# Kernel tuning notes

Hardware: AMD Instinct MI355X
Metric: run time of the kernel (lower is better)

Reference implementation:

```python
import jax, jax.numpy as jnp
import numpy as np

NUM_HEADS = 12
WINDOW = 128


def setup_inputs() -> dict:
    key = jax.random.key(0)
    k1, k2, k3, k4 = jax.random.split(key, 4)
    B, S, E = 2, 4096, 768
    x = jax.random.normal(k1, (B, S, E), dtype=jnp.float32)
    # nn.MultiheadAttention parameters
    w_in = jax.random.normal(k2, (3 * E, E), dtype=jnp.float32) * 0.02   # in_proj_weight
    b_in = jnp.zeros((3 * E,), dtype=jnp.float32)                        # in_proj_bias
    w_out = jax.random.normal(k3, (E, E), dtype=jnp.float32) * 0.02      # out_proj.weight
    b_out = jnp.zeros((E,), dtype=jnp.float32)                           # out_proj.bias
    return {"x": x, "w_in": w_in, "b_in": b_in, "w_out": w_out, "b_out": b_out}


def reference(x, w_in, b_in, w_out, b_out):
    B, S, E = x.shape
    H = NUM_HEADS
    D = E // H
    # fused qkv projection: x @ w_in.T + b_in -> [B, S, 3E]
    qkv = jnp.einsum('bse,fe->bsf', x, w_in) + b_in
    q, k, v = jnp.split(qkv, 3, axis=-1)
    q = q.reshape(B, S, H, D).transpose(0, 2, 1, 3)  # [B,H,S,D]
    k = k.reshape(B, S, H, D).transpose(0, 2, 1, 3)
    v = v.reshape(B, S, H, D).transpose(0, 2, 1, 3)
    scale = jnp.asarray(D, x.dtype) ** -0.5
    scores = jnp.einsum('bhqd,bhkd->bhqk', q * scale, k)  # [B,H,S,S]
    # Torch semantics: boolean attn_mask True == NOT allowed. The module sets
    # True inside the +-window band, so the band is masked out.
    idx = jnp.arange(S)
    band = jnp.abs(idx[:, None] - idx[None, :]) <= WINDOW  # True inside window
    scores = jnp.where(band[None, None, :, :], -jnp.inf, scores)
    attn = jax.nn.softmax(scores, axis=-1)
    out = jnp.einsum('bhqk,bhkd->bhqd', attn, v)  # [B,H,S,D]
    out = out.transpose(0, 2, 1, 3).reshape(B, S, E)
    return jnp.einsum('bse,fe->bsf', out, w_out) + b_out
```

## Files before the change

### kernel.cpp

```cpp
#include <hip/hip_runtime.h>
#include <hip/hip_bf16.h>
#include <stdint.h>

typedef __bf16 bf16_t;
typedef __bf16 bf16x8 __attribute__((ext_vector_type(8)));
typedef __bf16 bf16x4v __attribute__((ext_vector_type(4)));
typedef float f32x4 __attribute__((ext_vector_type(4)));

#define DEV __device__ __forceinline__

static constexpr int B_ = 2, S_ = 4096, E_ = 768, H_ = 12, D_ = 64;
static constexpr int WINDOW_ = 128;
static constexpr float QSCALE = 0.125f * 1.44269504088896f;

template<int C> struct IC { static constexpr int v = C; };

DEV float fexp2(float x) { return __builtin_amdgcn_exp2f(x); }

DEV void gload_lds16(const void* g, void* l) {
    __builtin_amdgcn_global_load_lds(
        (const __attribute__((address_space(1))) uint32_t*)g,
        (__attribute__((address_space(3))) uint32_t*)l, 16, 0, 0);
}

__global__ void k_cvt(const float* __restrict__ in, bf16_t* __restrict__ out, int n) {
    int i = (blockIdx.x * blockDim.x + threadIdx.x) * 4;
    if (i < n) {
        float4 v = *(const float4*)(in + i);
        bf16x4v o;
        o[0] = (bf16_t)v.x; o[1] = (bf16_t)v.y; o[2] = (bf16_t)v.z; o[3] = (bf16_t)v.w;
        *(bf16x4v*)(out + i) = o;
    }
}

template<int EPI>
__global__ void k_gemm(const bf16_t* __restrict__ A, const bf16_t* __restrict__ Bw,
                       const float* __restrict__ bias,
                       bf16_t* __restrict__ qb, bf16_t* __restrict__ kb, bf16_t* __restrict__ vtb,
                       float* __restrict__ outf,
                       int M, int N, int K, int mtiles) {
    __shared__ bf16_t As[128 * 64];
    __shared__ bf16_t Bs[128 * 64];
    int bid = blockIdx.x;
    int tm = bid % mtiles, tn = bid / mtiles;
    int m0 = tm * 128, n0 = tn * 128;
    int t = threadIdx.x;
    int lane = t & 63, wid = t >> 6;
    int l15 = lane & 15, l4 = lane >> 4;
    int wm = (wid & 1) * 64, wn = (wid >> 1) * 64;

    f32x4 acc[4][4];
#pragma unroll
    for (int i = 0; i < 4; ++i)
#pragma unroll
        for (int j = 0; j < 4; ++j) acc[i][j] = f32x4{0.f, 0.f, 0.f, 0.f};

    for (int kt = 0; kt < K; kt += 64) {
        __syncthreads();
#pragma unroll
        for (int c = 0; c < 4; ++c) {
            int idx = t + 256 * c;
            int row = idx >> 3, part = idx & 7;
            int kc = 8 * (part ^ (row & 7));
            gload_lds16(A + (long)(m0 + row) * K + kt + kc, (char*)As + idx * 16);
            gload_lds16(Bw + (long)(n0 + row) * K + kt + kc, (char*)Bs + idx * 16);
        }
        __syncthreads();
#pragma unroll
        for (int kk = 0; kk < 2; ++kk) {
            bf16x8 af[4], bfr[4];
#pragma unroll
            for (int i = 0; i < 4; ++i) {
                int row = wm + i * 16 + l15;
                int off = row * 128 + ((16 * (kk * 4 + l4)) ^ ((row & 7) << 4));
                af[i] = *(const bf16x8*)((const char*)As + off);
                int rowb = wn + i * 16 + l15;
                int offb = rowb * 128 + ((16 * (kk * 4 + l4)) ^ ((rowb & 7) << 4));
                bfr[i] = *(const bf16x8*)((const char*)Bs + offb);
            }
#pragma unroll
            for (int i = 0; i < 4; ++i)
#pragma unroll
                for (int j = 0; j < 4; ++j)
                    acc[i][j] = __builtin_amdgcn_mfma_f32_16x16x32_bf16(af[i], bfr[j], acc[i][j], 0, 0, 0);
        }
    }

#pragma unroll
    for (int i = 0; i < 4; ++i) {
#pragma unroll
        for (int j = 0; j < 4; ++j) {
            int n = n0 + wn + j * 16 + l15;
            float bv = bias[n];
            int mbase = m0 + wm + i * 16 + l4 * 4;
            if (EPI == 0) {
                int sel = n / 768, nn = n % 768;
                int h = nn >> 6, d = nn & 63;
                int b = mbase >> 12, s = mbase & 4095;
                if (sel == 2) {
                    bf16x4v pk;
#pragma unroll
                    for (int r = 0; r < 4; ++r) pk[r] = (bf16_t)(acc[i][j][r] + bv);
                    int pos = (s & ~31) | (((s >> 2) & 3) << 3) | (((s >> 4) & 1) << 2);
                    *(bf16x4v*)(vtb + ((long)(b * H_ + h) * D_ + d) * S_ + pos) = pk;
                } else {
                    long o = ((long)(b * H_ + h) * S_ + s) * D_ + d;
#pragma unroll
                    for (int r = 0; r < 4; ++r) {
                        float v = acc[i][j][r] + bv;
                        if (sel == 0) qb[o + (long)r * D_] = (bf16_t)(v * QSCALE);
                        else          kb[o + (long)r * D_] = (bf16_t)v;
                    }
                }
            } else {
#pragma unroll
                for (int r = 0; r < 4; ++r)
                    outf[(long)(mbase + r) * 768 + n] = acc[i][j][r] + bv;
            }
        }
    }
}

__global__ __launch_bounds__(512, 6)
void k_attn(const bf16_t* __restrict__ q, const bf16_t* __restrict__ k,
            const bf16_t* __restrict__ vt, bf16_t* __restrict__ ao) {
    __shared__ bf16_t Ksh[3][4096];
    __shared__ bf16_t Vsh[3][4096];
    int bid = blockIdx.x;
    bid = (bid & 7) * 96 + (bid >> 3);
    int bh = bid >> 5, qt = bid & 31;
    int q0 = qt * 128;
    int b = bh / H_, h = bh % H_;
    int t = threadIdx.x, lane = t & 63, wid = t >> 6;
    int l15 = lane & 15, l4 = lane >> 4;

    const bf16_t* qp = q + (long)bh * S_ * D_;
    const bf16_t* kp = k + (long)bh * S_ * D_;
    const bf16_t* vp = vt + (long)bh * D_ * S_;
    int wq = q0 + wid * 16;

    bf16x8 qf[2];
    {
        int row = wq + l15;
        qf[0] = *(const bf16x8*)(qp + (long)row * 64 + 8 * l4);
        qf[1] = *(const bf16x8*)(qp + (long)row * 64 + 32 + 8 * l4);
    }

    int sw = (l15 & 7) << 4;
    int a0 = l15 * 128 + ((16 * l4) ^ sw);
    int a1 = a0 ^ 64;

    f32x4 o[4], osum;
    osum = f32x4{0.f, 0.f, 0.f, 0.f};
#pragma unroll
    for (int ns = 0; ns < 4; ++ns) o[ns] = f32x4{0.f, 0.f, 0.f, 0.f};
    float m_ = 0.f;
    f32x4 mneg4 = f32x4{0.f, 0.f, 0.f, 0.f};

    bf16x8 onesB;
#pragma unroll
    for (int j = 0; j < 8; ++j) onesB[j] = (bf16_t)1.0f;

    int srow = t >> 3, spart = t & 7;
    int ssw = 8 * (spart ^ (srow & 7));
    int koff = srow * 64 + ssw;
    int voff = srow * S_ + ssw;
    int qt2 = 2 * qt;
    int qg = wq + l15;

    auto NK = [&](int i) { return i < qt2 ? i : i + 2; };

    auto STAGE = [&](int kts, auto bufc) {
        constexpr int buf = decltype(bufc)::v;
        gload_lds16(kp + ((long)kts << 12) + koff, (char*)Ksh + buf * 8192 + t * 16);
        gload_lds16(vp + (kts << 6) + voff, (char*)Vsh + buf * 8192 + t * 16);
    };

    auto QK = [&](auto curc, f32x4* s, f32x4 cinit) {
        constexpr int cur = decltype(curc)::v;
        const char* KL = (const char*)Ksh + cur * 8192;
#pragma unroll
        for (int ks = 0; ks < 4; ++ks) {
            bf16x8 kf0 = *(const bf16x8*)(KL + a0 + ks * 2048);
            bf16x8 kf1 = *(const bf16x8*)(KL + a1 + ks * 2048);
            s[ks] = __builtin_amdgcn_mfma_f32_16x16x32_bf16(kf0, qf[0], cinit, 0, 0, 0);
            s[ks] = __builtin_amdgcn_mfma_f32_16x16x32_bf16(kf1, qf[1], s[ks], 0, 0, 0);
        }
    };

    auto MASK = [&](int kt, f32x4* s) {
        int k0 = kt << 6;
#pragma unroll
        for (int ks = 0; ks < 4; ++ks) {
            int kb_ = k0 + ks * 16 + l4 * 4;
#pragma unroll
            for (int r = 0; r < 4; ++r) {
                int dd = qg - (kb_ + r); int ad = dd < 0 ? -dd : dd;
                if (ad <= WINDOW_) s[ks][r] = -1e30f;
            }
        }
    };

    auto TAIL = [&](auto curc, f32x4* s) {
        constexpr int cur = decltype(curc)::v;
        bf16x8 pa[2];
#pragma unroll
        for (int c = 0; c < 2; ++c) {
            pa[c][0] = (bf16_t)s[2*c][0];   pa[c][1] = (bf16_t)s[2*c][1];
            pa[c][2] = (bf16_t)s[2*c][2];   pa[c][3] = (bf16_t)s[2*c][3];
            pa[c][4] = (bf16_t)s[2*c+1][0]; pa[c][5] = (bf16_t)s[2*c+1][1];
            pa[c][6] = (bf16_t)s[2*c+1][2]; pa[c][7] = (bf16_t)s[2*c+1][3];
        }
        osum = __builtin_amdgcn_mfma_f32_16x16x32_bf16(pa[0], onesB, osum, 0, 0, 0);
        osum = __builtin_amdgcn_mfma_f32_16x16x32_bf16(pa[1], onesB, osum, 0, 0, 0);
        const char* VL = (const char*)Vsh + cur * 8192;
#pragma unroll
        for (int ns = 0; ns < 4; ++ns) {
            bf16x8 vf0 = *(const bf16x8*)(VL + a0 + ns * 2048);
            bf16x8 vf1 = *(const bf16x8*)(VL + a1 + ns * 2048);
            o[ns] = __builtin_amdgcn_mfma_f32_16x16x32_bf16(pa[0], vf0, o[ns], 0, 0, 0);
            o[ns] = __builtin_amdgcn_mfma_f32_16x16x32_bf16(pa[1], vf1, o[ns], 0, 0, 0);
        }
    };

    auto body = [&](int idx, auto curc) {
        if (idx < 61) {
            STAGE(NK(idx + 1), IC<(decltype(curc)::v + 1) % 3>{});
            asm volatile("s_waitcnt vmcnt(2)" ::: "memory");
        } else {
            asm volatile("s_waitcnt vmcnt(0)" ::: "memory");
        }
        __builtin_amdgcn_s_barrier();
        __builtin_amdgcn_sched_barrier(0);

        int kt = NK(idx);
        int dk = kt - qt2;
        f32x4 s[4];
        QK(curc, s, mneg4);
        if (dk == -2 || dk == -1 || dk == 2 || dk == 3) MASK(kt, s);
#pragma unroll
        for (int ks = 0; ks < 4; ++ks)
#pragma unroll
            for (int r = 0; r < 4; ++r)
                s[ks][r] = fexp2(s[ks][r]);
        TAIL(curc, s);
    };

    STAGE(NK(0), IC<0>{});

    {
        STAGE(NK(1), IC<1>{});
        asm volatile("s_waitcnt vmcnt(2)" ::: "memory");
        __builtin_amdgcn_s_barrier();
        __builtin_amdgcn_sched_barrier(0);

        int kt = NK(0);
        int dk = kt - qt2;
        f32x4 s[4];
        QK(IC<0>{}, s, f32x4{0.f, 0.f, 0.f, 0.f});
        if (dk == -2 || dk == -1 || dk == 2 || dk == 3) MASK(kt, s);
        float lm = -1e30f;
#pragma unroll
        for (int ks = 0; ks < 4; ++ks) {
            float a = fmaxf(fmaxf(s[ks][0], s[ks][1]), fmaxf(s[ks][2], s[ks][3]));
            lm = fmaxf(lm, a);
        }
        lm = fmaxf(lm, __shfl_xor(lm, 16));
        lm = fmaxf(lm, __shfl_xor(lm, 32));
        m_ = fmaxf(lm, 0.0f);
        mneg4 = f32x4{-m_, -m_, -m_, -m_};
#pragma unroll
        for (int ks = 0; ks < 4; ++ks)
#pragma unroll
            for (int r = 0; r < 4; ++r)
                s[ks][r] = fexp2(s[ks][r] - m_);
        TAIL(IC<0>{}, s);
    }

    for (int i3 = 0; i3 < 20; ++i3) {
        body(3 * i3 + 1, IC<1>{});
        body(3 * i3 + 2, IC<2>{});
        body(3 * i3 + 3, IC<0>{});
    }
    body(61, IC<1>{});

#pragma unroll
    for (int r = 0; r < 4; ++r) {
        float ir = 1.0f / osum[r];
        int srow2 = wq + l4 * 4 + r;
#pragma unroll
        for (int ns = 0; ns < 4; ++ns) {
            int e = h * 64 + ns * 16 + l15;
            ao[((long)b * S_ + srow2) * E_ + e] = (bf16_t)(o[ns][r] * ir);
        }
    }
}

extern "C" void kernel_launch(void* const* d_in, const int* in_sizes, int n_in,
                              void* d_out, int out_size, void* d_ws, size_t ws_size,
                              hipStream_t stream) {
    const float* x     = (const float*)d_in[0];
    const float* w_in  = (const float*)d_in[1];
    const float* b_in  = (const float*)d_in[2];
    const float* w_out = (const float*)d_in[3];
    const float* b_out = (const float*)d_in[4];
    float* out = (float*)d_out;

    char* ws = (char*)d_ws;
    bf16_t* xb  = (bf16_t*)(ws + 0);
    bf16_t* wib = (bf16_t*)(ws + 12582912);
    bf16_t* wob = (bf16_t*)(ws + 16121856);
    bf16_t* qb  = (bf16_t*)(ws + 17301504);
    bf16_t* kb  = (bf16_t*)(ws + 29884416);
    bf16_t* vtb = (bf16_t*)(ws + 42467328);
    bf16_t* ao  = xb;

    k_cvt<<<6144, 256, 0, stream>>>(x, xb, 6291456);
    k_cvt<<<1728, 256, 0, stream>>>(w_in, wib, 1769472);
    k_cvt<<<576, 256, 0, stream>>>(w_out, wob, 589824);

    k_gemm<0><<<64 * 18, 256, 0, stream>>>(xb, wib, b_in, qb, kb, vtb, nullptr,
                                           8192, 2304, 768, 64);
    k_attn<<<24 * 32, 512, 0, stream>>>(qb, kb, vtb, ao);
    k_gemm<1><<<64 * 6, 256, 0, stream>>>(ao, wob, b_out, nullptr, nullptr, nullptr, out,
                                          8192, 768, 768, 64);
}
```

Before: 189.9 us.

## Switch attention kernel to 32x32x16 MFMA with 4 waves and permlane swaps

Rewrites the windowed-attention kernel to use 32x32x16 bf16 MFMA tiles: each of 4 waves (256 threads) handles 32 query rows instead of 8 waves with 16 rows each. Score-to-P conversion uses permlane32_swap to reshape the accumulator into a B operand without going through LDS, and the V-transpose layout written by the QKV GEMM drops its permuted position encoding to match. The intent is fewer MFMA issues and fewer LDS reads per FLOP, plus vectorized output stores. The cost is higher register pressure from 16-wide accumulators and half the threads per block, each issuing twice the global-to-LDS loads.

Measured after the change: 207.8 us. 9.4% more time.

```diff
diff --git a/kernel.cpp b/kernel.cpp
--- a/kernel.cpp
+++ b/kernel.cpp
@@ -6,6 +6,7 @@
 typedef __bf16 bf16x8 __attribute__((ext_vector_type(8)));
 typedef __bf16 bf16x4v __attribute__((ext_vector_type(4)));
 typedef float f32x4 __attribute__((ext_vector_type(4)));
+typedef float f32x16 __attribute__((ext_vector_type(16)));
 
 #define DEV __device__ __forceinline__
 
@@ -16,6 +17,17 @@
 template<int C> struct IC { static constexpr int v = C; };
 
 DEV float fexp2(float x) { return __builtin_amdgcn_exp2f(x); }
+
+DEV uint32_t pk2(float lo, float hi) {
+    union { bf16_t h[2]; uint32_t u; } r;
+    r.h[0] = (bf16_t)lo; r.h[1] = (bf16_t)hi;
+    return r.u;
+}
+
+DEV void swap32(uint32_t& a, uint32_t& b) {
+    auto r = __builtin_amdgcn_permlane32_swap(a, b, false, false);
+    a = r[0]; b = r[1];
+}
 
 DEV void gload_lds16(const void* g, void* l) {
     __builtin_amdgcn_global_load_lds(
@@ -101,8 +113,7 @@
                     bf16x4v pk;
 #pragma unroll
                     for (int r = 0; r < 4; ++r) pk[r] = (bf16_t)(acc[i][j][r] + bv);
-                    int pos = (s & ~31) | (((s >> 2) & 3) << 3) | (((s >> 4) & 1) << 2);
-                    *(bf16x4v*)(vtb + ((long)(b * H_ + h) * D_ + d) * S_ + pos) = pk;
+                    *(bf16x4v*)(vtb + ((long)(b * H_ + h) * D_ + d) * S_ + s) = pk;
                 } else {
                     long o = ((long)(b * H_ + h) * S_ + s) * D_ + d;
 #pragma unroll
@@ -121,7 +132,7 @@
     }
 }
 
-__global__ __launch_bounds__(512, 6)
+__global__ __launch_bounds__(256, 3)
 void k_attn(const bf16_t* __restrict__ q, const bf16_t* __restrict__ k,
             const bf16_t* __restrict__ vt, bf16_t* __restrict__ ao) {
     __shared__ bf16_t Ksh[3][4096];
@@ -132,101 +143,103 @@
     int q0 = qt * 128;
     int b = bh / H_, h = bh % H_;
     int t = threadIdx.x, lane = t & 63, wid = t >> 6;
-    int l15 = lane & 15, l4 = lane >> 4;
+    int l31 = lane & 31, l5 = lane >> 5;
 
     const bf16_t* qp = q + (long)bh * S_ * D_;
     const bf16_t* kp = k + (long)bh * S_ * D_;
     const bf16_t* vp = vt + (long)bh * D_ * S_;
-    int wq = q0 + wid * 16;
-
-    bf16x8 qf[2];
-    {
-        int row = wq + l15;
-        qf[0] = *(const bf16x8*)(qp + (long)row * 64 + 8 * l4);
-        qf[1] = *(const bf16x8*)(qp + (long)row * 64 + 32 + 8 * l4);
-    }
-
-    int sw = (l15 & 7) << 4;
-    int a0 = l15 * 128 + ((16 * l4) ^ sw);
-    int a1 = a0 ^ 64;
-
-    f32x4 o[4], osum;
-    osum = f32x4{0.f, 0.f, 0.f, 0.f};
-#pragma unroll
-    for (int ns = 0; ns < 4; ++ns) o[ns] = f32x4{0.f, 0.f, 0.f, 0.f};
-    float m_ = 0.f;
-    f32x4 mneg4 = f32x4{0.f, 0.f, 0.f, 0.f};
-
-    bf16x8 onesB;
-#pragma unroll
-    for (int j = 0; j < 8; ++j) onesB[j] = (bf16_t)1.0f;
-
-    int srow = t >> 3, spart = t & 7;
-    int ssw = 8 * (spart ^ (srow & 7));
-    int koff = srow * 64 + ssw;
-    int voff = srow * S_ + ssw;
+    int wq = q0 + wid * 32;
+    int qg = wq + l31;
+
+    bf16x8 qf[4];
+#pragma unroll
+    for (int c = 0; c < 4; ++c)
+        qf[c] = *(const bf16x8*)(qp + (long)qg * 64 + 16 * c + 8 * l5);
+
+    int kofs[4];
+#pragma unroll
+    for (int c = 0; c < 4; ++c)
+        kofs[c] = l31 * 128 + 16 * (((c << 1) + l5) ^ (lane & 7));
+
+    f32x16 o0, o1, osum, mneg;
+#pragma unroll
+    for (int i = 0; i < 16; ++i) { o0[i] = 0.f; o1[i] = 0.f; osum[i] = 0.f; mneg[i] = 0.f; }
+
+    bf16x8 onesA;
+#pragma unroll
+    for (int j = 0; j < 8; ++j) onesA[j] = (bf16_t)1.0f;
+
+    int i2b = t + 256;
+    int rowA = t >> 3, rowB = i2b >> 3;
+    int koffA = rowA * 64 + 8 * ((t & 7) ^ (rowA & 7));
+    int koffB = rowB * 64 + 8 * ((i2b & 7) ^ (rowB & 7));
+    int voffA = rowA * S_ + 8 * ((t & 7) ^ (rowA & 7));
+    int voffB = rowB * S_ + 8 * ((i2b & 7) ^ (rowB & 7));
     int qt2 = 2 * qt;
-    int qg = wq + l15;
 
     auto NK = [&](int i) { return i < qt2 ? i : i + 2; };
 
     auto STAGE = [&](int kts, auto bufc) {
         constexpr int buf = decltype(bufc)::v;
-        gload_lds16(kp + ((long)kts << 12) + koff, (char*)Ksh + buf * 8192 + t * 16);
-        gload_lds16(vp + (kts << 6) + voff, (char*)Vsh + buf * 8192 + t * 16);
-    };
-
-    auto QK = [&](auto curc, f32x4* s, f32x4 cinit) {
+        char* Kd = (char*)Ksh + buf * 8192 + t * 16;
+        char* Vd = (char*)Vsh + buf * 8192 + t * 16;
+        long ko = (long)kts << 12;
+        int vo = kts << 6;
+        gload_lds16(kp + ko + koffA, Kd);
+        gload_lds16(kp + ko + koffB, Kd + 4096);
+        gload_lds16(vp + vo + voffA, Vd);
+        gload_lds16(vp + vo + voffB, Vd + 4096);
+    };
+
+    auto QKG = [&](const char* KL, const f32x16& ci) -> f32x16 {
+        f32x16 s;
+        bf16x8 kf = *(const bf16x8*)(KL + kofs[0]);
+        s = __builtin_amdgcn_mfma_f32_32x32x16_bf16(kf, qf[0], ci, 0, 0, 0);
+        kf = *(const bf16x8*)(KL + kofs[1]);
+        s = __builtin_amdgcn_mfma_f32_32x32x16_bf16(kf, qf[1], s, 0, 0, 0);
+        kf = *(const bf16x8*)(KL + kofs[2]);
+        s = __builtin_amdgcn_mfma_f32_32x32x16_bf16(kf, qf[2], s, 0, 0, 0);
+        kf = *(const bf16x8*)(KL + kofs[3]);
+        s = __builtin_amdgcn_mfma_f32_32x32x16_bf16(kf, qf[3], s, 0, 0, 0);
+        return s;
+    };
+
+    auto MASKG = [&](int kbase, f32x16& s) {
+#pragma unroll
+        for (int r = 0; r < 16; ++r) {
+            int key = kbase + (r & 3) + 8 * (r >> 2);
+            int dd = qg - key; int ad = dd < 0 ? -dd : dd;
+            if (ad <= WINDOW_) s[r] = -1e30f;
+        }
+    };
+
+    auto SMTAIL = [&](f32x16& s, const char* VL, auto cbc) {
+        constexpr int cb = decltype(cbc)::v;
+#pragma unroll
+        for (int r = 0; r < 16; ++r) s[r] = fexp2(s[r]);
+#pragma unroll
+        for (int cp = 0; cp < 2; ++cp) {
+            uint32_t x  = pk2(s[8 * cp + 0], s[8 * cp + 1]);
+            uint32_t y  = pk2(s[8 * cp + 2], s[8 * cp + 3]);
+            uint32_t x2 = pk2(s[8 * cp + 4], s[8 * cp + 5]);
+            uint32_t y2 = pk2(s[8 * cp + 6], s[8 * cp + 7]);
+            swap32(x, x2);
+            swap32(y, y2);
+            union { uint32_t u[4]; bf16x8 v; } pb;
+            pb.u[0] = x; pb.u[1] = y; pb.u[2] = x2; pb.u[3] = y2;
+            bf16x8 va0 = *(const bf16x8*)(VL + kofs[cb + cp]);
+            bf16x8 va1 = *(const bf16x8*)(VL + 4096 + kofs[cb + cp]);
+            o0   = __builtin_amdgcn_mfma_f32_32x32x16_bf16(va0, pb.v, o0, 0, 0, 0);
+            o1   = __builtin_amdgcn_mfma_f32_32x32x16_bf16(va1, pb.v, o1, 0, 0, 0);
+            osum = __builtin_amdgcn_mfma_f32_32x32x16_bf16(onesA, pb.v, osum, 0, 0, 0);
+        }
+    };
+
+    auto body = [&](int idx, auto curc) {
         constexpr int cur = decltype(curc)::v;
-        const char* KL = (const char*)Ksh + cur * 8192;
-#pragma unroll
-        for (int ks = 0; ks < 4; ++ks) {
-            bf16x8 kf0 = *(const bf16x8*)(KL + a0 + ks * 2048);
-            bf16x8 kf1 = *(const bf16x8*)(KL + a1 + ks * 2048);
-            s[ks] = __builtin_amdgcn_mfma_f32_16x16x32_bf16(kf0, qf[0], cinit, 0, 0, 0);
-            s[ks] = __builtin_amdgcn_mfma_f32_16x16x32_bf16(kf1, qf[1], s[ks], 0, 0, 0);
-        }
-    };
-
-    auto MASK = [&](int kt, f32x4* s) {
-        int k0 = kt << 6;
-#pragma unroll
-        for (int ks = 0; ks < 4; ++ks) {
-            int kb_ = k0 + ks * 16 + l4 * 4;
-#pragma unroll
-            for (int r = 0; r < 4; ++r) {
-                int dd = qg - (kb_ + r); int ad = dd < 0 ? -dd : dd;
-                if (ad <= WINDOW_) s[ks][r] = -1e30f;
-            }
-        }
-    };
-
-    auto TAIL = [&](auto curc, f32x4* s) {
-        constexpr int cur = decltype(curc)::v;
-        bf16x8 pa[2];
-#pragma unroll
-        for (int c = 0; c < 2; ++c) {
-            pa[c][0] = (bf16_t)s[2*c][0];   pa[c][1] = (bf16_t)s[2*c][1];
-            pa[c][2] = (bf16_t)s[2*c][2];   pa[c][3] = (bf16_t)s[2*c][3];
-            pa[c][4] = (bf16_t)s[2*c+1][0]; pa[c][5] = (bf16_t)s[2*c+1][1];
-            pa[c][6] = (bf16_t)s[2*c+1][2]; pa[c][7] = (bf16_t)s[2*c+1][3];
-        }
-        osum = __builtin_amdgcn_mfma_f32_16x16x32_bf16(pa[0], onesB, osum, 0, 0, 0);
-        osum = __builtin_amdgcn_mfma_f32_16x16x32_bf16(pa[1], onesB, osum, 0, 0, 0);
-        const char* VL = (const char*)Vsh + cur * 8192;
-#pragma unroll
-        for (int ns = 0; ns < 4; ++ns) {
-            bf16x8 vf0 = *(const bf16x8*)(VL + a0 + ns * 2048);
-            bf16x8 vf1 = *(const bf16x8*)(VL + a1 + ns * 2048);
-            o[ns] = __builtin_amdgcn_mfma_f32_16x16x32_bf16(pa[0], vf0, o[ns], 0, 0, 0);
-            o[ns] = __builtin_amdgcn_mfma_f32_16x16x32_bf16(pa[1], vf1, o[ns], 0, 0, 0);
-        }
-    };
-
-    auto body = [&](int idx, auto curc) {
         if (idx < 61) {
-            STAGE(NK(idx + 1), IC<(decltype(curc)::v + 1) % 3>{});
-            asm volatile("s_waitcnt vmcnt(2)" ::: "memory");
+            STAGE(NK(idx + 1), IC<(cur + 1) % 3>{});
+            asm volatile("s_waitcnt vmcnt(4)" ::: "memory");
         } else {
             asm volatile("s_waitcnt vmcnt(0)" ::: "memory");
         }
@@ -235,46 +248,52 @@
 
         int kt = NK(idx);
         int dk = kt - qt2;
-        f32x4 s[4];
-        QK(curc, s, mneg4);
-        if (dk == -2 || dk == -1 || dk == 2 || dk == 3) MASK(kt, s);
-#pragma unroll
-        for (int ks = 0; ks < 4; ++ks)
-#pragma unroll
-            for (int r = 0; r < 4; ++r)
-                s[ks][r] = fexp2(s[ks][r]);
-        TAIL(curc, s);
+        bool maskt = (dk == -2) | (dk == -1) | (dk == 2) | (dk == 3);
+        const char* KL = (const char*)Ksh + cur * 8192;
+        const char* VL = (const char*)Vsh + cur * 8192;
+
+        f32x16 s = QKG(KL, mneg);
+        if (maskt) MASKG((kt << 6) + 4 * l5, s);
+        SMTAIL(s, VL, IC<0>{});
+        f32x16 s2 = QKG(KL + 4096, mneg);
+        if (maskt) MASKG((kt << 6) + 32 + 4 * l5, s2);
+        SMTAIL(s2, VL, IC<2>{});
     };
 
     STAGE(NK(0), IC<0>{});
 
     {
         STAGE(NK(1), IC<1>{});
-        asm volatile("s_waitcnt vmcnt(2)" ::: "memory");
+        asm volatile("s_waitcnt vmcnt(4)" ::: "memory");
         __builtin_amdgcn_s_barrier();
         __builtin_amdgcn_sched_barrier(0);
 
         int kt = NK(0);
         int dk = kt - qt2;
-        f32x4 s[4];
-        QK(IC<0>{}, s, f32x4{0.f, 0.f, 0.f, 0.f});
-        if (dk == -2 || dk == -1 || dk == 2 || dk == 3) MASK(kt, s);
-        float lm = -1e30f;
-#pragma unroll
-        for (int ks = 0; ks < 4; ++ks) {
-            float a = fmaxf(fmaxf(s[ks][0], s[ks][1]), fmaxf(s[ks][2], s[ks][3]));
-            lm = fmaxf(lm, a);
-        }
-        lm = fmaxf(lm, __shfl_xor(lm, 16));
-        lm = fmaxf(lm, __shfl_xor(lm, 32));
-        m_ = fmaxf(lm, 0.0f);
-        mneg4 = f32x4{-m_, -m_, -m_, -m_};
-#pragma unroll
-        for (int ks = 0; ks < 4; ++ks)
-#pragma unroll
-            for (int r = 0; r < 4; ++r)
-                s[ks][r] = fexp2(s[ks][r] - m_);
-        TAIL(IC<0>{}, s);
+        bool maskt = (dk == -2) | (dk == -1) | (dk == 2) | (dk == 3);
+        const char* KL = (const char*)Ksh;
+        const char* VL = (const char*)Vsh;
+
+        f32x16 s = QKG(KL, mneg);
+        f32x16 s2 = QKG(KL + 4096, mneg);
+        if (maskt) { MASKG((kt << 6) + 4 * l5, s); MASKG((kt << 6) + 32 + 4 * l5, s2); }
+
+        float lm = s[0];
+#pragma unroll
+        for (int r = 1; r < 16; ++r) lm = fmaxf(lm, s[r]);
+#pragma unroll
+        for (int r = 0; r < 16; ++r) lm = fmaxf(lm, s2[r]);
+        union { float f; uint32_t u; } ua, ub;
+        ua.f = lm; ub.f = lm;
+        swap32(ua.u, ub.u);
+        lm = fmaxf(ua.f, ub.f);
+        float m_ = fmaxf(lm, 0.0f);
+#pragma unroll
+        for (int i = 0; i < 16; ++i) mneg[i] = -m_;
+#pragma unroll
+        for (int r = 0; r < 16; ++r) { s[r] -= m_; s2[r] -= m_; }
+        SMTAIL(s, VL, IC<0>{});
+        SMTAIL(s2, VL, IC<2>{});
     }
 
     for (int i3 = 0; i3 < 20; ++i3) {
@@ -284,14 +303,18 @@
     }
     body(61, IC<1>{});
 
-#pragma unroll
-    for (int r = 0; r < 4; ++r) {
-        float ir = 1.0f / osum[r];
-        int srow2 = wq + l4 * 4 + r;
-#pragma unroll
-        for (int ns = 0; ns < 4; ++ns) {
-            int e = h * 64 + ns * 16 + l15;
-            ao[((long)b * S_ + srow2) * E_ + e] = (bf16_t)(o[ns][r] * ir);
+    float inv = 1.0f / osum[0];
+    long baseo = ((long)b * S_ + qg) * E_ + h * 64;
+#pragma unroll
+    for (int dg = 0; dg < 2; ++dg) {
+        const f32x16& oo = dg ? o1 : o0;
+#pragma unroll
+        for (int rq = 0; rq < 4; ++rq) {
+            bf16x4v pk4;
+#pragma unroll
+            for (int j = 0; j < 4; ++j) pk4[j] = (bf16_t)(oo[rq * 4 + j] * inv);
+            int d = 8 * rq + 4 * l5 + 32 * dg;
+            *(bf16x4v*)(ao + baseo + d) = pk4;
         }
     }
 }
@@ -321,7 +344,7 @@
 
     k_gemm<0><<<64 * 18, 256, 0, stream>>>(xb, wib, b_in, qb, kb, vtb, nullptr,
                                            8192, 2304, 768, 64);
-    k_attn<<<24 * 32, 512, 0, stream>>>(qb, kb, vtb, ao);
+    k_attn<<<24 * 32, 256, 0, stream>>>(qb, kb, vtb, ao);
     k_gemm<1><<<64 * 6, 256, 0, stream>>>(ao, wob, b_out, nullptr, nullptr, nullptr, out,
                                           8192, 768, 768, 64);
 }
```

## Process two 16-row query groups per wave in attention kernel with 256 threads

Applied to the files above, without the earlier changes.

The attention kernel now uses 4 waves of 256 threads instead of 8 waves, and each wave handles 32 query rows as two 16-row groups. Every K and V fragment read from LDS is reused across both groups, which halves LDS read traffic per MFMA. Each thread issues twice as many global-to-LDS loads per stage, with the wait counts adjusted to match. The cost is more registers per wave (doubled accumulators and scores) and fewer waves per block to hide latency.

Result: faster. 184.5 us (-2.8%).

```diff
diff --git a/kernel.cpp b/kernel.cpp
--- a/kernel.cpp
+++ b/kernel.cpp
@@ -121,7 +121,7 @@
     }
 }
 
-__global__ __launch_bounds__(512, 6)
+__global__ __launch_bounds__(256, 3)
 void k_attn(const bf16_t* __restrict__ q, const bf16_t* __restrict__ k,
             const bf16_t* __restrict__ vt, bf16_t* __restrict__ ao) {
     __shared__ bf16_t Ksh[3][4096];
@@ -137,96 +137,121 @@
     const bf16_t* qp = q + (long)bh * S_ * D_;
     const bf16_t* kp = k + (long)bh * S_ * D_;
     const bf16_t* vp = vt + (long)bh * D_ * S_;
-    int wq = q0 + wid * 16;
-
-    bf16x8 qf[2];
-    {
-        int row = wq + l15;
-        qf[0] = *(const bf16x8*)(qp + (long)row * 64 + 8 * l4);
-        qf[1] = *(const bf16x8*)(qp + (long)row * 64 + 32 + 8 * l4);
+    int wq = q0 + wid * 32;
+
+    bf16x8 qf[2][2];
+#pragma unroll
+    for (int g = 0; g < 2; ++g) {
+        int row = wq + g * 16 + l15;
+        qf[g][0] = *(const bf16x8*)(qp + (long)row * 64 + 8 * l4);
+        qf[g][1] = *(const bf16x8*)(qp + (long)row * 64 + 32 + 8 * l4);
     }
 
     int sw = (l15 & 7) << 4;
     int a0 = l15 * 128 + ((16 * l4) ^ sw);
     int a1 = a0 ^ 64;
 
-    f32x4 o[4], osum;
-    osum = f32x4{0.f, 0.f, 0.f, 0.f};
-#pragma unroll
-    for (int ns = 0; ns < 4; ++ns) o[ns] = f32x4{0.f, 0.f, 0.f, 0.f};
-    float m_ = 0.f;
-    f32x4 mneg4 = f32x4{0.f, 0.f, 0.f, 0.f};
+    f32x4 o[2][4], osum[2];
+    f32x4 mneg4[2];
+#pragma unroll
+    for (int g = 0; g < 2; ++g) {
+        osum[g] = f32x4{0.f, 0.f, 0.f, 0.f};
+        mneg4[g] = f32x4{0.f, 0.f, 0.f, 0.f};
+#pragma unroll
+        for (int ns = 0; ns < 4; ++ns) o[g][ns] = f32x4{0.f, 0.f, 0.f, 0.f};
+    }
 
     bf16x8 onesB;
 #pragma unroll
     for (int j = 0; j < 8; ++j) onesB[j] = (bf16_t)1.0f;
 
-    int srow = t >> 3, spart = t & 7;
-    int ssw = 8 * (spart ^ (srow & 7));
-    int koff = srow * 64 + ssw;
-    int voff = srow * S_ + ssw;
+    int i2b = t + 256;
+    int rowA = t >> 3, rowB = i2b >> 3;
+    int part = t & 7;
+    int koffA = rowA * 64 + 8 * (part ^ (rowA & 7));
+    int koffB = rowB * 64 + 8 * (part ^ (rowB & 7));
+    int voffA = rowA * S_ + 8 * (part ^ (rowA & 7));
+    int voffB = rowB * S_ + 8 * (part ^ (rowB & 7));
     int qt2 = 2 * qt;
-    int qg = wq + l15;
+    int qg0 = wq + l15;
+    int qg1 = qg0 + 16;
 
     auto NK = [&](int i) { return i < qt2 ? i : i + 2; };
 
     auto STAGE = [&](int kts, auto bufc) {
         constexpr int buf = decltype(bufc)::v;
-        gload_lds16(kp + ((long)kts << 12) + koff, (char*)Ksh + buf * 8192 + t * 16);
-        gload_lds16(vp + (kts << 6) + voff, (char*)Vsh + buf * 8192 + t * 16);
-    };
-
-    auto QK = [&](auto curc, f32x4* s, f32x4 cinit) {
+        char* Kd = (char*)Ksh + buf * 8192 + t * 16;
+        char* Vd = (char*)Vsh + buf * 8192 + t * 16;
+        long ko = (long)kts << 12;
+        int vo = kts << 6;
+        gload_lds16(kp + ko + koffA, Kd);
+        gload_lds16(kp + ko + koffB, Kd + 4096);
+        gload_lds16(vp + vo + voffA, Vd);
+        gload_lds16(vp + vo + voffB, Vd + 4096);
+    };
+
+    auto QK = [&](auto curc, f32x4 (*s)[4], f32x4 ci0, f32x4 ci1) {
         constexpr int cur = decltype(curc)::v;
         const char* KL = (const char*)Ksh + cur * 8192;
 #pragma unroll
         for (int ks = 0; ks < 4; ++ks) {
             bf16x8 kf0 = *(const bf16x8*)(KL + a0 + ks * 2048);
             bf16x8 kf1 = *(const bf16x8*)(KL + a1 + ks * 2048);
-            s[ks] = __builtin_amdgcn_mfma_f32_16x16x32_bf16(kf0, qf[0], cinit, 0, 0, 0);
-            s[ks] = __builtin_amdgcn_mfma_f32_16x16x32_bf16(kf1, qf[1], s[ks], 0, 0, 0);
-        }
-    };
-
-    auto MASK = [&](int kt, f32x4* s) {
+            s[0][ks] = __builtin_amdgcn_mfma_f32_16x16x32_bf16(kf0, qf[0][0], ci0, 0, 0, 0);
+            s[1][ks] = __builtin_amdgcn_mfma_f32_16x16x32_bf16(kf0, qf[1][0], ci1, 0, 0, 0);
+            s[0][ks] = __builtin_amdgcn_mfma_f32_16x16x32_bf16(kf1, qf[0][1], s[0][ks], 0, 0, 0);
+            s[1][ks] = __builtin_amdgcn_mfma_f32_16x16x32_bf16(kf1, qf[1][1], s[1][ks], 0, 0, 0);
+        }
+    };
+
+    auto MASK = [&](int kt, f32x4 (*s)[4]) {
         int k0 = kt << 6;
 #pragma unroll
         for (int ks = 0; ks < 4; ++ks) {
             int kb_ = k0 + ks * 16 + l4 * 4;
 #pragma unroll
             for (int r = 0; r < 4; ++r) {
-                int dd = qg - (kb_ + r); int ad = dd < 0 ? -dd : dd;
-                if (ad <= WINDOW_) s[ks][r] = -1e30f;
-            }
-        }
-    };
-
-    auto TAIL = [&](auto curc, f32x4* s) {
+                int d0 = qg0 - (kb_ + r); int ad0 = d0 < 0 ? -d0 : d0;
+                if (ad0 <= WINDOW_) s[0][ks][r] = -1e30f;
+                int d1 = qg1 - (kb_ + r); int ad1 = d1 < 0 ? -d1 : d1;
+                if (ad1 <= WINDOW_) s[1][ks][r] = -1e30f;
+            }
+        }
+    };
+
+    auto TAIL = [&](auto curc, f32x4 (*s)[4]) {
         constexpr int cur = decltype(curc)::v;
-        bf16x8 pa[2];
-#pragma unroll
-        for (int c = 0; c < 2; ++c) {
-            pa[c][0] = (bf16_t)s[2*c][0];   pa[c][1] = (bf16_t)s[2*c][1];
-            pa[c][2] = (bf16_t)s[2*c][2];   pa[c][3] = (bf16_t)s[2*c][3];
-            pa[c][4] = (bf16_t)s[2*c+1][0]; pa[c][5] = (bf16_t)s[2*c+1][1];
-            pa[c][6] = (bf16_t)s[2*c+1][2]; pa[c][7] = (bf16_t)s[2*c+1][3];
-        }
-        osum = __builtin_amdgcn_mfma_f32_16x16x32_bf16(pa[0], onesB, osum, 0, 0, 0);
-        osum = __builtin_amdgcn_mfma_f32_16x16x32_bf16(pa[1], onesB, osum, 0, 0, 0);
+        bf16x8 pa[2][2];
+#pragma unroll
+        for (int g = 0; g < 2; ++g)
+#pragma unroll
+            for (int c = 0; c < 2; ++c) {
+                pa[g][c][0] = (bf16_t)s[g][2*c][0];   pa[g][c][1] = (bf16_t)s[g][2*c][1];
+                pa[g][c][2] = (bf16_t)s[g][2*c][2];   pa[g][c][3] = (bf16_t)s[g][2*c][3];
+                pa[g][c][4] = (bf16_t)s[g][2*c+1][0]; pa[g][c][5] = (bf16_t)s[g][2*c+1][1];
+                pa[g][c][6] = (bf16_t)s[g][2*c+1][2]; pa[g][c][7] = (bf16_t)s[g][2*c+1][3];
+            }
+#pragma unroll
+        for (int g = 0; g < 2; ++g) {
+            osum[g] = __builtin_amdgcn_mfma_f32_16x16x32_bf16(pa[g][0], onesB, osum[g], 0, 0, 0);
+            osum[g] = __builtin_amdgcn_mfma_f32_16x16x32_bf16(pa[g][1], onesB, osum[g], 0, 0, 0);
+        }
         const char* VL = (const char*)Vsh + cur * 8192;
 #pragma unroll
         for (int ns = 0; ns < 4; ++ns) {
             bf16x8 vf0 = *(const bf16x8*)(VL + a0 + ns * 2048);
             bf16x8 vf1 = *(const bf16x8*)(VL + a1 + ns * 2048);
-            o[ns] = __builtin_amdgcn_mfma_f32_16x16x32_bf16(pa[0], vf0, o[ns], 0, 0, 0);
-            o[ns] = __builtin_amdgcn_mfma_f32_16x16x32_bf16(pa[1], vf1, o[ns], 0, 0, 0);
+            o[0][ns] = __builtin_amdgcn_mfma_f32_16x16x32_bf16(pa[0][0], vf0, o[0][ns], 0, 0, 0);
+            o[1][ns] = __builtin_amdgcn_mfma_f32_16x16x32_bf16(pa[1][0], vf0, o[1][ns], 0, 0, 0);
+            o[0][ns] = __builtin_amdgcn_mfma_f32_16x16x32_bf16(pa[0][1], vf1, o[0][ns], 0, 0, 0);
+            o[1][ns] = __builtin_amdgcn_mfma_f32_16x16x32_bf16(pa[1][1], vf1, o[1][ns], 0, 0, 0);
         }
     };
 
     auto body = [&](int idx, auto curc) {
         if (idx < 61) {
             STAGE(NK(idx + 1), IC<(decltype(curc)::v + 1) % 3>{});
-            asm volatile("s_waitcnt vmcnt(2)" ::: "memory");
+            asm volatile("s_waitcnt vmcnt(4)" ::: "memory");
         } else {
             asm volatile("s_waitcnt vmcnt(0)" ::: "memory");
         }
@@ -235,14 +260,16 @@
 
         int kt = NK(idx);
         int dk = kt - qt2;
-        f32x4 s[4];
-        QK(curc, s, mneg4);
+        f32x4 s[2][4];
+        QK(curc, s, mneg4[0], mneg4[1]);
         if (dk == -2 || dk == -1 || dk == 2 || dk == 3) MASK(kt, s);
 #pragma unroll
-        for (int ks = 0; ks < 4; ++ks)
-#pragma unroll
-            for (int r = 0; r < 4; ++r)
-                s[ks][r] = fexp2(s[ks][r]);
+        for (int g = 0; g < 2; ++g)
+#pragma unroll
+            for (int ks = 0; ks < 4; ++ks)
+#pragma unroll
+                for (int r = 0; r < 4; ++r)
+                    s[g][ks][r] = fexp2(s[g][ks][r]);
         TAIL(curc, s);
     };
 
@@ -250,30 +277,33 @@
 
     {
         STAGE(NK(1), IC<1>{});
-        asm volatile("s_waitcnt vmcnt(2)" ::: "memory");
+        asm volatile("s_waitcnt vmcnt(4)" ::: "memory");
         __builtin_amdgcn_s_barrier();
         __builtin_amdgcn_sched_barrier(0);
 
         int kt = NK(0);
         int dk = kt - qt2;
-        f32x4 s[4];
-        QK(IC<0>{}, s, f32x4{0.f, 0.f, 0.f, 0.f});
+        f32x4 s[2][4];
+        QK(IC<0>{}, s, f32x4{0.f,0.f,0.f,0.f}, f32x4{0.f,0.f,0.f,0.f});
         if (dk == -2 || dk == -1 || dk == 2 || dk == 3) MASK(kt, s);
-        float lm = -1e30f;
-#pragma unroll
-        for (int ks = 0; ks < 4; ++ks) {
-            float a = fmaxf(fmaxf(s[ks][0], s[ks][1]), fmaxf(s[ks][2], s[ks][3]));
-            lm = fmaxf(lm, a);
-        }
-        lm = fmaxf(lm, __shfl_xor(lm, 16));
-        lm = fmaxf(lm, __shfl_xor(lm, 32));
-        m_ = fmaxf(lm, 0.0f);
-        mneg4 = f32x4{-m_, -m_, -m_, -m_};
-#pragma unroll
-        for (int ks = 0; ks < 4; ++ks)
-#pragma unroll
-            for (int r = 0; r < 4; ++r)
-                s[ks][r] = fexp2(s[ks][r] - m_);
+#pragma unroll
+        for (int g = 0; g < 2; ++g) {
+            float lm = -1e30f;
+#pragma unroll
+            for (int ks = 0; ks < 4; ++ks) {
+                float a = fmaxf(fmaxf(s[g][ks][0], s[g][ks][1]), fmaxf(s[g][ks][2], s[g][ks][3]));
+                lm = fmaxf(lm, a);
+            }
+            lm = fmaxf(lm, __shfl_xor(lm, 16));
+            lm = fmaxf(lm, __shfl_xor(lm, 32));
+            float m_ = fmaxf(lm, 0.0f);
+            mneg4[g] = f32x4{-m_, -m_, -m_, -m_};
+#pragma unroll
+            for (int ks = 0; ks < 4; ++ks)
+#pragma unroll
+                for (int r = 0; r < 4; ++r)
+                    s[g][ks][r] = fexp2(s[g][ks][r] - m_);
+        }
         TAIL(IC<0>{}, s);
     }
 
@@ -285,15 +315,17 @@
     body(61, IC<1>{});
 
 #pragma unroll
-    for (int r = 0; r < 4; ++r) {
-        float ir = 1.0f / osum[r];
-        int srow2 = wq + l4 * 4 + r;
-#pragma unroll
-        for (int ns = 0; ns < 4; ++ns) {
-            int e = h * 64 + ns * 16 + l15;
-            ao[((long)b * S_ + srow2) * E_ + e] = (bf16_t)(o[ns][r] * ir);
-        }
-    }
+    for (int g = 0; g < 2; ++g)
+#pragma unroll
+        for (int r = 0; r < 4; ++r) {
+            float ir = 1.0f / osum[g][r];
+            int srow2 = wq + g * 16 + l4 * 4 + r;
+#pragma unroll
+            for (int ns = 0; ns < 4; ++ns) {
+                int e = h * 64 + ns * 16 + l15;
+                ao[((long)b * S_ + srow2) * E_ + e] = (bf16_t)(o[g][ns][r] * ir);
+            }
+        }
 }
 
 extern "C" void kernel_launch(void* const* d_in, const int* in_sizes, int n_in,
@@ -321,7 +353,7 @@
 
     k_gemm<0><<<64 * 18, 256, 0, stream>>>(xb, wib, b_in, qb, kb, vtb, nullptr,
                                            8192, 2304, 768, 64);
-    k_attn<<<24 * 32, 512, 0, stream>>>(qb, kb, vtb, ao);
+    k_attn<<<24 * 32, 256, 0, stream>>>(qb, kb, vtb, ao);
     k_gemm<1><<<64 * 6, 256, 0, stream>>>(ao, wob, b_out, nullptr, nullptr, nullptr, out,
                                           8192, 768, 768, 64);
 }
```
